# Kernel optimization log

Measured on AMD Instinct MI355X. Metric: run time of the kernel, lower is better.

The kernel has to match this reference:

```python
import jax, jax.numpy as jnp
import numpy as np

N_ANGLES = 64      # init kwarg n_angles
PAD_RATIO = 1.0    # init kwarg pad_ratio


def setup_inputs() -> dict:
    key = jax.random.key(0)
    x = jax.random.normal(key, (4, 1, 384, 384), dtype=jnp.float32)
    return {"x": x}


def _radon(x):
    B, _, H, W = x.shape
    pad = int(PAD_RATIO * 0.1 * min(H, W))
    xp = jnp.pad(x, ((0, 0), (0, 0), (pad, pad), (pad, pad)))
    Hp, Wp = xp.shape[2], xp.shape[3]
    img = xp[:, 0]  # (B, Hp, Wp)

    # angles: linspace(0, 180, n+1)[:-1], degrees -> radians
    angles = jnp.linspace(0.0, 180.0, N_ANGLES + 1)[:-1]
    th = angles * (jnp.pi / 180.0)
    c, s = jnp.cos(th), jnp.sin(th)  # (A,)

    # F.affine_grid(align_corners=False): normalized output coords at pixel centers
    xs = (2.0 * jnp.arange(Wp, dtype=jnp.float32) + 1.0) / Wp - 1.0  # (Wp,)
    ys = (2.0 * jnp.arange(Hp, dtype=jnp.float32) + 1.0) / Hp - 1.0  # (Hp,)
    # rot = [[c,-s,0],[s,c,0]] applied to (x_out, y_out, 1)
    gx = c[:, None, None] * xs[None, None, :] - s[:, None, None] * ys[None, :, None]  # (A,Hp,Wp)
    gy = s[:, None, None] * xs[None, None, :] + c[:, None, None] * ys[None, :, None]

    # grid_sample(align_corners=False): map normalized -> input pixel coords
    ix = ((gx + 1.0) * Wp - 1.0) * 0.5
    iy = ((gy + 1.0) * Hp - 1.0) * 0.5
    ix0f = jnp.floor(ix)
    iy0f = jnp.floor(iy)
    wx = ix - ix0f  # (A,Hp,Wp)
    wy = iy - iy0f
    ix0 = ix0f.astype(jnp.int32)
    iy0 = iy0f.astype(jnp.int32)

    def gather(iyc, ixc):
        # zeros padding: out-of-range taps contribute 0
        valid = (ixc >= 0) & (ixc < Wp) & (iyc >= 0) & (iyc < Hp)
        iyc_c = jnp.clip(iyc, 0, Hp - 1)
        ixc_c = jnp.clip(ixc, 0, Wp - 1)
        v = img[:, iyc_c, ixc_c]  # (B, A, Hp, Wp)
        return v * valid[None].astype(img.dtype)

    v00 = gather(iy0, ix0)
    v01 = gather(iy0, ix0 + 1)
    v10 = gather(iy0 + 1, ix0)
    v11 = gather(iy0 + 1, ix0 + 1)

    sampled = (v00 * ((1.0 - wy) * (1.0 - wx))[None]
               + v01 * ((1.0 - wy) * wx)[None]
               + v10 * (wy * (1.0 - wx))[None]
               + v11 * (wy * wx)[None])  # (B, A, Hp, Wp)

    proj = sampled.sum(axis=3) / Wp  # (B, A, Hp)
    return jnp.transpose(proj, (0, 2, 1))  # (B, Hp, A)


def reference(x):
    return _radon(x)
```

## Files before the change

### kernel.cpp

```cpp
#include <hip/hip_runtime.h>
#include <hip/hip_bf16.h>


constexpr int IMG = 384;
constexpr int PAD = 38;
constexpr int P   = 460;
constexpr int NA  = 64;
constexpr int NB  = 4;
constexpr int B_  = 6;
constexpr int O_  = PAD - B_;
constexpr int E_  = IMG + 2 * B_;

__device__ __forceinline__ unsigned int f2bfu(float f) {
    __hip_bfloat16 h = __float2bfloat16(f);
    return (unsigned int)__builtin_bit_cast(unsigned short, h);
}
__device__ __forceinline__ float bf_lo(unsigned int w) { return __uint_as_float(w << 16); }
__device__ __forceinline__ float bf_hi(unsigned int w) { return __uint_as_float(w & 0xffff0000u); }

__global__ __launch_bounds__(256) void pad4_kernel(const float* __restrict__ x,
                                                   uint2* __restrict__ pb,
                                                   uint2* __restrict__ pbT) {
    __shared__ uint2 tile[64][65];
    const int tx = threadIdx.x;
    const int ty = threadIdx.y;
    const int bx = blockIdx.x * 64;
    const int by = blockIdx.y * 64;

    for (int r = ty; r < 64; r += 4) {
        const int iy = by + r, ix = bx + tx;
        const int py = iy - B_, px = ix - B_;
        uint2 t = make_uint2(0u, 0u);
        if ((unsigned)py < (unsigned)IMG && (unsigned)px < (unsigned)IMG) {
            const int o = py * IMG + px;
            t.x = f2bfu(x[o])                 | (f2bfu(x[IMG * IMG + o])     << 16);
            t.y = f2bfu(x[2 * IMG * IMG + o]) | (f2bfu(x[3 * IMG * IMG + o]) << 16);
        }
        tile[r][tx] = t;
        if (iy < E_ && ix < E_) pb[iy * E_ + ix] = t;
    }
    __syncthreads();
    for (int r = ty; r < 64; r += 4) {
        const int oy = bx + r;
        const int ox = by + tx;
        if (oy < E_ && ox < E_) pbT[oy * E_ + ox] = tile[tx][r];
    }
}

__global__ __launch_bounds__(128) void radon_kernel(const uint2* __restrict__ pb,
                                                    const uint2* __restrict__ pbT,
                                                    float* __restrict__ out) {
    const int lane = threadIdx.x & 63;
    const int wv   = threadIdx.x >> 6;
    const int l    = lane & 15;
    const int g    = lane >> 4;
    const int a    = blockIdx.y;
    const int y    = blockIdx.x * 8 + wv * 4 + g;

    const float th = (2.8125f * (float)a) * 0.017453292519943295f;
    float s, c;
    __sincosf(th, &s, &c);

    const float yf = (float)(y < P ? y : P - 1);
    const float ys = (2.0f * yf + 1.0f) / 460.0f - 1.0f;
    const float A  = fmaf(-s, ys, 1.0f) * 230.0f - 0.5f - 229.5f * c;
    const float By = fmaf( c, ys, 1.0f) * 230.0f - 0.5f - 229.5f * s;

    const float rc = __builtin_amdgcn_rcpf(c);
    const float rs = __builtin_amdgcn_rcpf(s);
    float t0 = (36.0f - A) * rc, t1 = (424.0f - A) * rc;
    float lo = fmaxf(0.0f,   fminf(t0, t1));
    float hi = fminf(459.0f, fmaxf(t0, t1));
    t0 = (36.0f - By) * rs; t1 = (424.0f - By) * rs;
    lo = fmaxf(lo, fminf(t0, t1));
    hi = fminf(hi, fmaxf(t0, t1));

    int glo = max(0, (int)floorf(lo) - 2);
    glo = min(glo, P);
    int ghi = min(P - 1, (int)ceilf(hi) + 2);
    if (y >= P) { glo = 1; ghi = 0; }

    const bool  useT = fabsf(s) > fabsf(c);
    const float cu = useT ? s  : c;
    const float Au = useT ? By : A;
    const float cv = useT ? c  : s;
    const float Av = useT ? A  : By;
    const uint2* __restrict__ base = useT ? pbT : pb;

    float acc0 = 0.0f, acc1 = 0.0f, acc2 = 0.0f, acc3 = 0.0f;
    float xxf = (float)(glo + l);
    #pragma unroll 2
    for (int xx = glo + l; xx <= ghi; xx += 16, xxf += 16.0f) {
        const float u   = fmaf(cu, xxf, Au);
        const float v   = fmaf(cv, xxf, Av);
        const float u0f = floorf(u);
        const float v0f = floorf(v);
        const float wu  = u - u0f;
        const float wvv = v - v0f;
        const int idx = (int)fmaf(v0f, (float)E_, u0f) - (O_ * E_ + O_);

        const uint2* p = base + idx;
        const uint2 T00 = p[0];
        const uint2 T01 = p[1];
        const uint2 T10 = p[E_];
        const uint2 T11 = p[E_ + 1];

        {
            const float top = fmaf(wu, bf_lo(T01.x) - bf_lo(T00.x), bf_lo(T00.x));
            const float bot = fmaf(wu, bf_lo(T11.x) - bf_lo(T10.x), bf_lo(T10.x));
            acc0 += fmaf(wvv, bot - top, top);
        }
        {
            const float top = fmaf(wu, bf_hi(T01.x) - bf_hi(T00.x), bf_hi(T00.x));
            const float bot = fmaf(wu, bf_hi(T11.x) - bf_hi(T10.x), bf_hi(T10.x));
            acc1 += fmaf(wvv, bot - top, top);
        }
        {
            const float top = fmaf(wu, bf_lo(T01.y) - bf_lo(T00.y), bf_lo(T00.y));
            const float bot = fmaf(wu, bf_lo(T11.y) - bf_lo(T10.y), bf_lo(T10.y));
            acc2 += fmaf(wvv, bot - top, top);
        }
        {
            const float top = fmaf(wu, bf_hi(T01.y) - bf_hi(T00.y), bf_hi(T00.y));
            const float bot = fmaf(wu, bf_hi(T11.y) - bf_hi(T10.y), bf_hi(T10.y));
            acc3 += fmaf(wvv, bot - top, top);
        }
    }

    #pragma unroll
    for (int m = 1; m <= 8; m <<= 1) {
        acc0 += __shfl_xor(acc0, m);
        acc1 += __shfl_xor(acc1, m);
        acc2 += __shfl_xor(acc2, m);
        acc3 += __shfl_xor(acc3, m);
    }

    if (l == 0 && y < P) {
        out[(0 * P + y) * NA + a] = acc0 / 460.0f;
        out[(1 * P + y) * NA + a] = acc1 / 460.0f;
        out[(2 * P + y) * NA + a] = acc2 / 460.0f;
        out[(3 * P + y) * NA + a] = acc3 / 460.0f;
    }
}

__device__ __forceinline__ float samp(const float* __restrict__ img, int iy, int ix) {
    unsigned uy = (unsigned)(iy - PAD);
    unsigned ux = (unsigned)(ix - PAD);
    return (uy < (unsigned)IMG && ux < (unsigned)IMG) ? img[uy * IMG + ux] : 0.0f;
}

__global__ __launch_bounds__(256) void radon_fallback(const float* __restrict__ x,
                                                      float* __restrict__ out) {
    const int wid  = blockIdx.x * 4 + (threadIdx.x >> 6);
    const int lane = threadIdx.x & 63;
    if (wid >= NB * NA * P) return;
    const int y  = wid % P;
    const int ba = wid / P;
    const int a  = ba % NA;
    const int b  = ba / NA;
    const float th = (2.8125f * (float)a) * 0.017453292519943295f;
    float s, c;
    __sincosf(th, &s, &c);
    const float ysy = (2.0f * (float)y + 1.0f) / 460.0f - 1.0f;
    const float* img = x + b * IMG * IMG;
    float acc = 0.0f;
    for (int xx = lane; xx < P; xx += 64) {
        const float xsx = (2.0f * (float)xx + 1.0f) / 460.0f - 1.0f;
        const float gx = c * xsx - s * ysy;
        const float gy = s * xsx + c * ysy;
        const float fix = ((gx + 1.0f) * 460.0f - 1.0f) * 0.5f;
        const float fiy = ((gy + 1.0f) * 460.0f - 1.0f) * 0.5f;
        const float ix0f = floorf(fix);
        const float iy0f = floorf(fiy);
        const float wx = fix - ix0f;
        const float wy = fiy - iy0f;
        const int ix0 = (int)ix0f;
        const int iy0 = (int)iy0f;
        const float v00 = samp(img, iy0,     ix0);
        const float v01 = samp(img, iy0,     ix0 + 1);
        const float v10 = samp(img, iy0 + 1, ix0);
        const float v11 = samp(img, iy0 + 1, ix0 + 1);
        acc += v00 * ((1.0f - wy) * (1.0f - wx))
             + v01 * ((1.0f - wy) * wx)
             + v10 * (wy * (1.0f - wx))
             + v11 * (wy * wx);
    }
    #pragma unroll
    for (int off = 32; off; off >>= 1) acc += __shfl_xor(acc, off);
    if (lane == 0) out[(b * P + y) * NA + a] = acc / 460.0f;
}

extern "C" void kernel_launch(void* const* d_in, const int* in_sizes, int n_in,
                              void* d_out, int out_size, void* d_ws, size_t ws_size,
                              hipStream_t stream) {
    const float* x = (const float*)d_in[0];
    float* out = (float*)d_out;

    const size_t layer = (size_t)E_ * E_;
    const size_t need  = 2 * layer * sizeof(uint2);

    if (ws_size >= need) {
        uint2* pb  = (uint2*)d_ws;
        uint2* pbT = pb + layer;
        dim3 pgrid((E_ + 63) / 64, (E_ + 63) / 64);
        pad4_kernel<<<pgrid, dim3(64, 4), 0, stream>>>(x, pb, pbT);
        dim3 grid((P + 7) / 8, NA);
        radon_kernel<<<grid, 128, 0, stream>>>(pb, pbT, out);
    } else {
        const int total_waves = NB * NA * P;
        const int blocks = (total_waves + 3) / 4;
        radon_fallback<<<blocks, 256, 0, stream>>>(x, out);
    }
}
```

Baseline: 31.95 us.

## Flatten pad kernel and fetch bilinear taps as 16-byte vector loads

The pad/transpose kernel drops its shared-memory tiled transpose and becomes a flat one-thread-per-pixel kernel that writes both layouts directly, so the transposed store is strided and uncoalesced. The radon inner loop replaces four 8-byte tap loads with two 16-byte loads covering adjacent pixel pairs, which halves the load instruction count. The wide loads can be misaligned because idx is arbitrary, which may split accesses or cost extra on some paths. The uncoalesced transposed writes in the preprocessing kernel may add cost.

```diff
diff --git a/kernel.cpp b/kernel.cpp
--- a/kernel.cpp
+++ b/kernel.cpp
@@ -21,30 +21,19 @@
 __global__ __launch_bounds__(256) void pad4_kernel(const float* __restrict__ x,
                                                    uint2* __restrict__ pb,
                                                    uint2* __restrict__ pbT) {
-    __shared__ uint2 tile[64][65];
-    const int tx = threadIdx.x;
-    const int ty = threadIdx.y;
-    const int bx = blockIdx.x * 64;
-    const int by = blockIdx.y * 64;
-
-    for (int r = ty; r < 64; r += 4) {
-        const int iy = by + r, ix = bx + tx;
-        const int py = iy - B_, px = ix - B_;
-        uint2 t = make_uint2(0u, 0u);
-        if ((unsigned)py < (unsigned)IMG && (unsigned)px < (unsigned)IMG) {
-            const int o = py * IMG + px;
-            t.x = f2bfu(x[o])                 | (f2bfu(x[IMG * IMG + o])     << 16);
-            t.y = f2bfu(x[2 * IMG * IMG + o]) | (f2bfu(x[3 * IMG * IMG + o]) << 16);
-        }
-        tile[r][tx] = t;
-        if (iy < E_ && ix < E_) pb[iy * E_ + ix] = t;
-    }
-    __syncthreads();
-    for (int r = ty; r < 64; r += 4) {
-        const int oy = bx + r;
-        const int ox = by + tx;
-        if (oy < E_ && ox < E_) pbT[oy * E_ + ox] = tile[tx][r];
-    }
+    const int idx = blockIdx.x * 256 + threadIdx.x;
+    if (idx >= E_ * E_) return;
+    const int iy = idx / E_;
+    const int ix = idx - iy * E_;
+    const int py = iy - B_, px = ix - B_;
+    uint2 t = make_uint2(0u, 0u);
+    if ((unsigned)py < (unsigned)IMG && (unsigned)px < (unsigned)IMG) {
+        const int o = py * IMG + px;
+        t.x = f2bfu(x[o])                 | (f2bfu(x[IMG * IMG + o])     << 16);
+        t.y = f2bfu(x[2 * IMG * IMG + o]) | (f2bfu(x[3 * IMG * IMG + o]) << 16);
+    }
+    pb[iy * E_ + ix]  = t;
+    pbT[ix * E_ + iy] = t;
 }
 
 __global__ __launch_bounds__(128) void radon_kernel(const uint2* __restrict__ pb,
@@ -99,30 +88,27 @@
         const float wvv = v - v0f;
         const int idx = (int)fmaf(v0f, (float)E_, u0f) - (O_ * E_ + O_);
 
-        const uint2* p = base + idx;
-        const uint2 T00 = p[0];
-        const uint2 T01 = p[1];
-        const uint2 T10 = p[E_];
-        const uint2 T11 = p[E_ + 1];
-
-        {
-            const float top = fmaf(wu, bf_lo(T01.x) - bf_lo(T00.x), bf_lo(T00.x));
-            const float bot = fmaf(wu, bf_lo(T11.x) - bf_lo(T10.x), bf_lo(T10.x));
+        const uint4 R0 = *reinterpret_cast<const uint4*>(base + idx);
+        const uint4 R1 = *reinterpret_cast<const uint4*>(base + idx + E_);
+
+        {
+            const float top = fmaf(wu, bf_lo(R0.z) - bf_lo(R0.x), bf_lo(R0.x));
+            const float bot = fmaf(wu, bf_lo(R1.z) - bf_lo(R1.x), bf_lo(R1.x));
             acc0 += fmaf(wvv, bot - top, top);
         }
         {
-            const float top = fmaf(wu, bf_hi(T01.x) - bf_hi(T00.x), bf_hi(T00.x));
-            const float bot = fmaf(wu, bf_hi(T11.x) - bf_hi(T10.x), bf_hi(T10.x));
+            const float top = fmaf(wu, bf_hi(R0.z) - bf_hi(R0.x), bf_hi(R0.x));
+            const float bot = fmaf(wu, bf_hi(R1.z) - bf_hi(R1.x), bf_hi(R1.x));
             acc1 += fmaf(wvv, bot - top, top);
         }
         {
-            const float top = fmaf(wu, bf_lo(T01.y) - bf_lo(T00.y), bf_lo(T00.y));
-            const float bot = fmaf(wu, bf_lo(T11.y) - bf_lo(T10.y), bf_lo(T10.y));
+            const float top = fmaf(wu, bf_lo(R0.w) - bf_lo(R0.y), bf_lo(R0.y));
+            const float bot = fmaf(wu, bf_lo(R1.w) - bf_lo(R1.y), bf_lo(R1.y));
             acc2 += fmaf(wvv, bot - top, top);
         }
         {
-            const float top = fmaf(wu, bf_hi(T01.y) - bf_hi(T00.y), bf_hi(T00.y));
-            const float bot = fmaf(wu, bf_hi(T11.y) - bf_hi(T10.y), bf_hi(T10.y));
+            const float top = fmaf(wu, bf_hi(R0.w) - bf_hi(R0.y), bf_hi(R0.y));
+            const float bot = fmaf(wu, bf_hi(R1.w) - bf_hi(R1.y), bf_hi(R1.y));
             acc3 += fmaf(wvv, bot - top, top);
         }
     }
@@ -202,8 +188,8 @@
     if (ws_size >= need) {
         uint2* pb  = (uint2*)d_ws;
         uint2* pbT = pb + layer;
-        dim3 pgrid((E_ + 63) / 64, (E_ + 63) / 64);
-        pad4_kernel<<<pgrid, dim3(64, 4), 0, stream>>>(x, pb, pbT);
+        const int pad_blocks = (E_ * E_ + 255) / 256;
+        pad4_kernel<<<pad_blocks, 256, 0, stream>>>(x, pb, pbT);
         dim3 grid((P + 7) / 8, NA);
         radon_kernel<<<grid, 128, 0, stream>>>(pb, pbT, out);
     } else {
```

Result: faster. 28.77 us, median of 2 (-10.0%).
